# Optimization experiments

Measured on AMD Instinct MI355X. Metric: run time of the kernel, lower is better.

Reference implementation:

```python
import jax, jax.numpy as jnp
import numpy as np

B, S, IN_F, OUT_F = 4, 2048, 4096, 4096
ALPHA = 0.01

def setup_inputs() -> dict:
    key = jax.random.key(0)
    k1, k2 = jax.random.split(key, 2)
    # int8-valued activations and weights (stored as int32 per harness dtype)
    x = jax.random.randint(k1, (B, S, IN_F), -127, 127, dtype=jnp.int32)
    weight = jax.random.randint(k2, (IN_F, OUT_F), -127, 127, dtype=jnp.int32)
    bias = jnp.zeros((1, OUT_F), dtype=jnp.float16)
    alpha = jnp.full((1,), ALPHA, dtype=jnp.float32)
    return {"x": x, "weight": weight, "bias": bias, "alpha": alpha}

def reference(x, weight, bias, alpha):
    # Faithful to forward's default (non-hybrid) path:
    # y = F.linear(x.float(), weight.t().float(), bias.float()) * alpha
    # F.linear(x, W^T) == x @ W, with W shape (in_features, out_features).
    x_shape = x.shape
    xf = x.reshape(-1, x_shape[-1]).astype(jnp.float32)          # [B*S, in]
    wf = weight.astype(jnp.float32)                               # [in, out]
    y = (xf @ wf + bias.astype(jnp.float32)) * alpha              # [B*S, out]
    return y.reshape(*x_shape[:-1], -1)                           # [B, S, out]
```

## Files before the change

kernel.cpp:

```cpp
#include <hip/hip_runtime.h>
#include <hip/hip_fp16.h>

using i32x4  = __attribute__((ext_vector_type(4)))  int;
using i32x16 = __attribute__((ext_vector_type(16))) int;

static constexpr int M  = 4 * 2048;
static constexpr int N  = 4096;
static constexpr int K  = 4096;
static constexpr int NT = K / 64;
static constexpr int ATILE = 256 * 64;
static constexpr int BTILE = 128 * 64;

static constexpr int PX_BLOCKS = (int)((size_t)M * K / 16 / 256);
static constexpr int PW_BLOCKS = (int)((size_t)N * K / 16 / 256);

__device__ __forceinline__ unsigned pack4(i32x4 v) {
  return (unsigned)((v.x & 255) | ((v.y & 255) << 8) | ((v.z & 255) << 16) | (v.w << 24));
}

__global__ __launch_bounds__(256) void pack_kernel(const int* __restrict__ x,
                                                   const int* __restrict__ w,
                                                   unsigned char* __restrict__ wa,
                                                   unsigned char* __restrict__ wb) {
  if (blockIdx.x < PX_BLOCKS) {
    unsigned g = blockIdx.x * 256 + threadIdx.x;
    unsigned row = g & 255;
    unsigned kg  = (g >> 8) & 3;
    unsigned kt  = (g >> 10) & 63;
    unsigned br  = g >> 16;
    const int* src = x + ((size_t)(br * 256 + row) * K + kt * 64 + kg * 16);
    i32x4 v0 = *(const i32x4*)(src + 0);
    i32x4 v1 = *(const i32x4*)(src + 4);
    i32x4 v2 = *(const i32x4*)(src + 8);
    i32x4 v3 = *(const i32x4*)(src + 12);
    i32x4 d;
    d.x = (int)pack4(v0); d.y = (int)pack4(v1); d.z = (int)pack4(v2); d.w = (int)pack4(v3);
    *(i32x4*)(wa + (size_t)g * 16) = d;
  } else {
    unsigned g = (blockIdx.x - PX_BLOCKS) * 256 + threadIdx.x;
    unsigned col = g & 127;
    unsigned kg  = (g >> 7) & 3;
    unsigned kt  = (g >> 9) & 63;
    unsigned bn  = g >> 15;
    unsigned n   = bn * 128 + col;
    unsigned k0  = kt * 64 + kg * 16;
    const int* src = w + (size_t)k0 * N + n;
    i32x4 d;
#pragma unroll
    for (int j = 0; j < 4; ++j) {
      int b0 = src[(size_t)(j * 4 + 0) * N];
      int b1 = src[(size_t)(j * 4 + 1) * N];
      int b2 = src[(size_t)(j * 4 + 2) * N];
      int b3 = src[(size_t)(j * 4 + 3) * N];
      d[j] = (b0 & 255) | ((b1 & 255) << 8) | ((b2 & 255) << 16) | (b3 << 24);
    }
    *(i32x4*)(wb + (size_t)g * 16) = d;
  }
}


__device__ __forceinline__ void gload_lds16(const void* g, void* l) {
  __builtin_amdgcn_global_load_lds((const __attribute__((address_space(1))) unsigned int*)g,
                                   (__attribute__((address_space(3))) unsigned int*)l,
                                   16, 0, 0);
}

#define FENCE()   asm volatile("" ::: "memory")
#define BARRIER() do { FENCE(); __builtin_amdgcn_s_barrier(); FENCE(); } while (0)

__global__ __launch_bounds__(768, 3) void gemm_i8(const unsigned char* __restrict__ wa,
                                                  const unsigned char* __restrict__ wb,
                                                  const __half* __restrict__ bias,
                                                  const float* __restrict__ alphaP,
                                                  float* __restrict__ out) {
  __shared__ __align__(16) unsigned char As[3][ATILE];

  const int tid  = threadIdx.x;
  const int lane = tid & 63;
  const int w    = tid >> 6;
  const int l31  = lane & 31;
  const int kgl  = lane >> 5;

  const int bc = blockIdx.x;
  const int br = blockIdx.y;

  const unsigned char* ga = wa + (size_t)br * NT * ATILE;

  if (w >= 8) {
    const int pw = w - 8;
    const int poff = pw * 4096;

#define STAGE(T) do {                                                          \
      const unsigned char* src = ga + (size_t)(T) * ATILE + poff + lane * 16;  \
      unsigned char* dst = &As[(T) % 3][poff];                                 \
      gload_lds16(src +    0, dst +    0);                                     \
      gload_lds16(src + 1024, dst + 1024);                                     \
      gload_lds16(src + 2048, dst + 2048);                                     \
      gload_lds16(src + 3072, dst + 3072);                                     \
    } while (0)

    STAGE(0);
    STAGE(1);
    asm volatile("s_waitcnt vmcnt(4)" ::: "memory");
    BARRIER();
    for (int t = 0; t < NT; ++t) {
      if (t + 2 < NT) STAGE(t + 2);
      if (t + 2 < NT)      asm volatile("s_waitcnt vmcnt(4)" ::: "memory");
      else if (t + 1 < NT) asm volatile("s_waitcnt vmcnt(0)" ::: "memory");
      BARRIER();
    }
#undef STAGE
    return;
  }

  const int cr = w >> 1, cc = w & 1;
  const int arow = cr * 64 + l31;
  const int bcol = cc * 64 + l31;

  const unsigned char* gbw = wb + (size_t)bc * NT * BTILE;

  i32x4 b[2][2][2];
  i32x16 acc[2][2] = {};

#define BLOAD(PAR, T) do {                                                     \
    const unsigned char* bt = gbw + (size_t)(T) * BTILE;                       \
    b[PAR][0][0] = *(const i32x4*)(bt + (kgl)     * 2048 + (bcol +  0) * 16);  \
    b[PAR][0][1] = *(const i32x4*)(bt + (kgl)     * 2048 + (bcol + 32) * 16);  \
    b[PAR][1][0] = *(const i32x4*)(bt + (2 + kgl) * 2048 + (bcol +  0) * 16);  \
    b[PAR][1][1] = *(const i32x4*)(bt + (2 + kgl) * 2048 + (bcol + 32) * 16);  \
  } while (0)

#define CHUNK(SLOT, KC, PAR) do {                                              \
    const unsigned char* Ap = (SLOT) + ((KC) * 2 + kgl) * 4096;                \
    i32x4 a0 = *(const i32x4*)(Ap + (arow +  0) * 16);                         \
    i32x4 a1 = *(const i32x4*)(Ap + (arow + 32) * 16);                         \
    acc[0][0] = __builtin_amdgcn_mfma_i32_32x32x32_i8(a0, b[PAR][KC][0], acc[0][0], 0, 0, 0); \
    acc[0][1] = __builtin_amdgcn_mfma_i32_32x32x32_i8(a0, b[PAR][KC][1], acc[0][1], 0, 0, 0); \
    acc[1][0] = __builtin_amdgcn_mfma_i32_32x32x32_i8(a1, b[PAR][KC][0], acc[1][0], 0, 0, 0); \
    acc[1][1] = __builtin_amdgcn_mfma_i32_32x32x32_i8(a1, b[PAR][KC][1], acc[1][1], 0, 0, 0); \
  } while (0)

#define CSTEP(T, PAR) do {                                                     \
    if ((T) + 1 < NT) BLOAD(PAR ^ 1, (T) + 1);    \
    const unsigned char* slot = &As[(T) % 3][0];                               \
    __builtin_amdgcn_s_setprio(1);                                             \
    CHUNK(slot, 0, PAR);                                                       \
    CHUNK(slot, 1, PAR);                                                       \
    __builtin_amdgcn_s_setprio(0);                                             \
    BARRIER();                                                                 \
  } while (0)

  BLOAD(0, 0);
  BARRIER();
  for (int t = 0; t < NT; t += 2) {
    CSTEP(t, 0);
    CSTEP(t + 1, 1);
  }

  const float alpha = *alphaP;
  const int row0 = br * 256 + cr * 64 + 4 * kgl;
  const int col0 = bc * 128 + cc * 64 + l31;
#pragma unroll
  for (int ni = 0; ni < 2; ++ni) {
    const int col = col0 + ni * 32;
    const float bf = __half2float(bias[col]);
#pragma unroll
    for (int mi = 0; mi < 2; ++mi) {
#pragma unroll
      for (int r = 0; r < 16; ++r) {
        const int row = row0 + mi * 32 + (r & 3) + 8 * (r >> 2);
        out[(size_t)row * N + col] = ((float)acc[mi][ni][r] + bf) * alpha;
      }
    }
  }
#undef CSTEP
#undef CHUNK
#undef BLOAD
}

extern "C" void kernel_launch(void* const* d_in, const int* in_sizes, int n_in,
                              void* d_out, int out_size, void* d_ws, size_t ws_size,
                              hipStream_t stream) {
  const int*    x     = (const int*)d_in[0];
  const int*    wgt   = (const int*)d_in[1];
  const __half* bias  = (const __half*)d_in[2];
  const float*  alpha = (const float*)d_in[3];
  float*        out   = (float*)d_out;

  unsigned char* wa = (unsigned char*)d_ws;
  unsigned char* wb = wa + (size_t)M * K;

  pack_kernel<<<PX_BLOCKS + PW_BLOCKS, 256, 0, stream>>>(x, wgt, wa, wb);

  dim3 grid(N / 128, M / 256);
  gemm_i8<<<grid, 768, 0, stream>>>(wa, wb, bias, alpha, out);
}
```

Baseline: 244.5 us.

## Use 4 compute waves with 128x64 subtiles and 4-tile LDS super-stages

The block drops from 12 to 8 waves (4 compute, 4 producer). Each compute wave now covers 128 rows instead of 64, so every B register load feeds twice as many MFMAs. The producer stages 256 K-values (64KB) per double-buffered stage, which cuts barriers to one per four K-tiles. In exchange, LDS use rises to 128KB, occupancy drops to one block per CU, and prefetch depth within a stage is reduced. Each wave also holds more accumulator registers.

```diff
diff --git a/kernel.cpp b/kernel.cpp
--- a/kernel.cpp
+++ b/kernel.cpp
@@ -8,6 +8,7 @@
 static constexpr int N  = 4096;
 static constexpr int K  = 4096;
 static constexpr int NT = K / 64;
+static constexpr int NS = K / 256;
 static constexpr int ATILE = 256 * 64;
 static constexpr int BTILE = 128 * 64;
 
@@ -68,16 +69,17 @@
 #define FENCE()   asm volatile("" ::: "memory")
 #define BARRIER() do { FENCE(); __builtin_amdgcn_s_barrier(); FENCE(); } while (0)
 
-__global__ __launch_bounds__(768, 3) void gemm_i8(const unsigned char* __restrict__ wa,
+__global__ __launch_bounds__(512, 1) void gemm_i8(const unsigned char* __restrict__ wa,
                                                   const unsigned char* __restrict__ wb,
                                                   const __half* __restrict__ bias,
                                                   const float* __restrict__ alphaP,
                                                   float* __restrict__ out) {
-  __shared__ __align__(16) unsigned char As[3][ATILE];
+  __shared__ __align__(16) unsigned char As[2][65536];
 
   const int tid  = threadIdx.x;
   const int lane = tid & 63;
   const int w    = tid >> 6;
+  const int cw   = w & 3;
   const int l31  = lane & 31;
   const int kgl  = lane >> 5;
 
@@ -86,41 +88,39 @@
 
   const unsigned char* ga = wa + (size_t)br * NT * ATILE;
 
-  if (w >= 8) {
-    const int pw = w - 8;
-    const int poff = pw * 4096;
-
-#define STAGE(T) do {                                                          \
-      const unsigned char* src = ga + (size_t)(T) * ATILE + poff + lane * 16;  \
-      unsigned char* dst = &As[(T) % 3][poff];                                 \
-      gload_lds16(src +    0, dst +    0);                                     \
-      gload_lds16(src + 1024, dst + 1024);                                     \
-      gload_lds16(src + 2048, dst + 2048);                                     \
-      gload_lds16(src + 3072, dst + 3072);                                     \
+  if (w >= 4) {
+    const int poff = cw * 16384;
+
+#define STAGE(S) do {                                                          \
+      const unsigned char* src = ga + (size_t)(S) * 65536 + poff + lane * 16;  \
+      unsigned char* dst = &As[(S) & 1][poff];                                 \
+      _Pragma("unroll")                                                        \
+      for (int j = 0; j < 16; ++j)                                             \
+        gload_lds16(src + j * 1024, dst + j * 1024);                           \
     } while (0)
 
     STAGE(0);
-    STAGE(1);
-    asm volatile("s_waitcnt vmcnt(4)" ::: "memory");
+    asm volatile("s_waitcnt vmcnt(0)" ::: "memory");
     BARRIER();
-    for (int t = 0; t < NT; ++t) {
-      if (t + 2 < NT) STAGE(t + 2);
-      if (t + 2 < NT)      asm volatile("s_waitcnt vmcnt(4)" ::: "memory");
-      else if (t + 1 < NT) asm volatile("s_waitcnt vmcnt(0)" ::: "memory");
+    for (int s = 0; s < NS; ++s) {
+      if (s + 1 < NS) {
+        STAGE(s + 1);
+        asm volatile("s_waitcnt vmcnt(0)" ::: "memory");
+      }
       BARRIER();
     }
 #undef STAGE
     return;
   }
 
-  const int cr = w >> 1, cc = w & 1;
-  const int arow = cr * 64 + l31;
+  const int cr = cw >> 1, cc = cw & 1;
+  const int arow = cr * 128 + l31;
   const int bcol = cc * 64 + l31;
 
   const unsigned char* gbw = wb + (size_t)bc * NT * BTILE;
 
   i32x4 b[2][2][2];
-  i32x16 acc[2][2] = {};
+  i32x16 acc[4][2] = {};
 
 #define BLOAD(PAR, T) do {                                                     \
     const unsigned char* bt = gbw + (size_t)(T) * BTILE;                       \
@@ -130,42 +130,51 @@
     b[PAR][1][1] = *(const i32x4*)(bt + (2 + kgl) * 2048 + (bcol + 32) * 16);  \
   } while (0)
 
-#define CHUNK(SLOT, KC, PAR) do {                                              \
-    const unsigned char* Ap = (SLOT) + ((KC) * 2 + kgl) * 4096;                \
+#define CHUNK(TOFF, KC, PAR) do {                                              \
+    const unsigned char* Ap = slot + (TOFF) + ((KC) * 2 + kgl) * 4096;         \
     i32x4 a0 = *(const i32x4*)(Ap + (arow +  0) * 16);                         \
     i32x4 a1 = *(const i32x4*)(Ap + (arow + 32) * 16);                         \
+    i32x4 a2 = *(const i32x4*)(Ap + (arow + 64) * 16);                         \
+    i32x4 a3 = *(const i32x4*)(Ap + (arow + 96) * 16);                         \
     acc[0][0] = __builtin_amdgcn_mfma_i32_32x32x32_i8(a0, b[PAR][KC][0], acc[0][0], 0, 0, 0); \
     acc[0][1] = __builtin_amdgcn_mfma_i32_32x32x32_i8(a0, b[PAR][KC][1], acc[0][1], 0, 0, 0); \
     acc[1][0] = __builtin_amdgcn_mfma_i32_32x32x32_i8(a1, b[PAR][KC][0], acc[1][0], 0, 0, 0); \
     acc[1][1] = __builtin_amdgcn_mfma_i32_32x32x32_i8(a1, b[PAR][KC][1], acc[1][1], 0, 0, 0); \
+    acc[2][0] = __builtin_amdgcn_mfma_i32_32x32x32_i8(a2, b[PAR][KC][0], acc[2][0], 0, 0, 0); \
+    acc[2][1] = __builtin_amdgcn_mfma_i32_32x32x32_i8(a2, b[PAR][KC][1], acc[2][1], 0, 0, 0); \
+    acc[3][0] = __builtin_amdgcn_mfma_i32_32x32x32_i8(a3, b[PAR][KC][0], acc[3][0], 0, 0, 0); \
+    acc[3][1] = __builtin_amdgcn_mfma_i32_32x32x32_i8(a3, b[PAR][KC][1], acc[3][1], 0, 0, 0); \
   } while (0)
 
-#define CSTEP(T, PAR) do {                                                     \
-    if ((T) + 1 < NT) BLOAD(PAR ^ 1, (T) + 1);    \
-    const unsigned char* slot = &As[(T) % 3][0];                               \
+#define TILE_J(S, J) do {                                                      \
+    const int tt = (S) * 4 + (J);                                              \
+    if (tt + 1 < NT) BLOAD(((J) + 1) & 1, tt + 1);                             \
     __builtin_amdgcn_s_setprio(1);                                             \
-    CHUNK(slot, 0, PAR);                                                       \
-    CHUNK(slot, 1, PAR);                                                       \
+    CHUNK((J) * 16384, 0, (J) & 1);                                            \
+    CHUNK((J) * 16384, 1, (J) & 1);                                            \
     __builtin_amdgcn_s_setprio(0);                                             \
-    BARRIER();                                                                 \
   } while (0)
 
   BLOAD(0, 0);
   BARRIER();
-  for (int t = 0; t < NT; t += 2) {
-    CSTEP(t, 0);
-    CSTEP(t + 1, 1);
+  for (int s = 0; s < NS; ++s) {
+    const unsigned char* slot = &As[s & 1][0];
+    TILE_J(s, 0);
+    TILE_J(s, 1);
+    TILE_J(s, 2);
+    TILE_J(s, 3);
+    BARRIER();
   }
 
   const float alpha = *alphaP;
-  const int row0 = br * 256 + cr * 64 + 4 * kgl;
+  const int row0 = br * 256 + cr * 128 + 4 * kgl;
   const int col0 = bc * 128 + cc * 64 + l31;
 #pragma unroll
   for (int ni = 0; ni < 2; ++ni) {
     const int col = col0 + ni * 32;
     const float bf = __half2float(bias[col]);
 #pragma unroll
-    for (int mi = 0; mi < 2; ++mi) {
+    for (int mi = 0; mi < 4; ++mi) {
 #pragma unroll
       for (int r = 0; r < 16; ++r) {
         const int row = row0 + mi * 32 + (r & 3) + 8 * (r >> 2);
@@ -173,7 +182,7 @@
       }
     }
   }
-#undef CSTEP
+#undef TILE_J
 #undef CHUNK
 #undef BLOAD
 }
@@ -193,5 +202,5 @@
   pack_kernel<<<PX_BLOCKS + PW_BLOCKS, 256, 0, stream>>>(x, wgt, wa, wb);
 
   dim3 grid(N / 128, M / 256);
-  gemm_i8<<<grid, 768, 0, stream>>>(wa, wb, bias, alpha, out);
-}
+  gemm_i8<<<grid, 512, 0, stream>>>(wa, wb, bias, alpha, out);
+}
```

After: 225.0 us. 8.0% less time.
